# Kernel tuning notes

Measured on AMD Instinct MI355X. Metric: run time of the kernel, lower is better.

## Reference

```python
import jax, jax.numpy as jnp
import numpy as np
import math

F = 64        # num_features (multiplicity of each irrep)
N = 16000     # nodes
E = 256000    # edges (avg_num_neighbors = 16)
S = 4         # num_species
DE = 32       # scalar edge feature dim (radial basis)
W = 128       # interaction_mlp_width
AVG_NEIGH = 16.0
SQ2 = math.sqrt(2.0)
SQ3 = math.sqrt(3.0)


def setup_inputs() -> dict:
    key = jax.random.key(0)
    ks = jax.random.split(key, 32)
    def nrm(k, shape, scale=1.0):
        return jax.random.normal(k, shape, dtype=jnp.float32) * scale
    inp = {}
    # forward args
    inp["vectors"] = nrm(ks[0], (E, 1, 3))
    inp["lengths"] = jax.random.uniform(ks[1], (E, 1), dtype=jnp.float32)
    inp["node_s"] = nrm(ks[2], (N, F))            # 64x0e part of node_feats
    inp["node_v"] = nrm(ks[3], (N, F, 3))         # 64x1o part of node_feats
    inp["scalar_edge_feats"] = nrm(ks[4], (E, DE))
    inp["node_specie"] = jax.random.randint(ks[5], (N,), 0, S)
    inp["senders"] = jax.random.randint(ks[6], (E,), 0, N)
    inp["receivers"] = jax.random.randint(ks[7], (E,), 0, N)
    # parameters (e3nn Linear = per-irrep channel mixing, fan-in normalized; bias only on 0e)
    inp["W_up_s"] = nrm(ks[8], (F, F), F ** -0.5); inp["b_up_s"] = jnp.zeros((F,), jnp.float32)
    inp["W_up_v"] = nrm(ks[9], (F, F), F ** -0.5)
    din = 2 * F + DE + 1
    inp["mlp_W1"] = nrm(ks[10], (din, W), din ** -0.5); inp["mlp_b1"] = jnp.zeros((W,), jnp.float32)
    inp["mlp_W2"] = nrm(ks[11], (W, W), W ** -0.5); inp["mlp_b2"] = jnp.zeros((W,), jnp.float32)
    inp["mlp_W3"] = nrm(ks[12], (W, 3 * F), W ** -0.5); inp["mlp_b3"] = jnp.zeros((3 * F,), jnp.float32)
    inp["W_dn_s"] = nrm(ks[13], (F, F), F ** -0.5); inp["b_dn_s"] = jnp.zeros((F,), jnp.float32)
    inp["W_dn_v"] = nrm(ks[14], (2 * F, F), (2 * F) ** -0.5)
    # symmetric contraction weights (per species, per channel); correlation=2
    inp["w_sc_s"] = nrm(ks[15], (S, 3, F), 3 ** -0.5)   # paths to 0e: x0, x0^2, (x1.x1)/sqrt3
    inp["w_sc_v"] = nrm(ks[16], (S, 2, F), 2 ** -0.5)   # paths to 1o: x1, x0*x1
    inp["W_pb_s"] = nrm(ks[17], (F, F), F ** -0.5); inp["b_pb_s"] = jnp.zeros((F,), jnp.float32)
    inp["W_pb_v"] = nrm(ks[18], (F, F), F ** -0.5)
    inp["W_r1_s"] = nrm(ks[19], (F, 2 * F), F ** -0.5); inp["b_r1_s"] = jnp.zeros((2 * F,), jnp.float32)
    inp["W_r1_v"] = nrm(ks[20], (F, F), F ** -0.5)
    inp["W_r2_s"] = nrm(ks[21], (F, 1), F ** -0.5); inp["b_r2"] = jnp.zeros((1,), jnp.float32)
    inp["W_r2_v"] = nrm(ks[22], (F, 1), F ** -0.5)
    return inp


def reference(vectors, lengths, node_s, node_v, scalar_edge_feats, node_specie,
              senders, receivers,
              W_up_s, b_up_s, W_up_v,
              mlp_W1, mlp_b1, mlp_W2, mlp_b2, mlp_W3, mlp_b3,
              W_dn_s, b_dn_s, W_dn_v,
              w_sc_s, w_sc_v, W_pb_s, b_pb_s, W_pb_v,
              W_r1_s, b_r1_s, W_r1_v, W_r2_s, b_r2, W_r2_v):
    n = node_s.shape[0]
    # --- spherical harmonics, sh_irreps='1o', component normalization, normalize=False ---
    edge_v = SQ3 * vectors[:, 0, :]                              # [E,3]

    # --- InteractionBlock: linear_up ---
    h_s = node_s @ W_up_s + b_up_s                               # [N,F]
    h_v = jnp.einsum('nfi,fg->ngi', node_v, W_up_v)              # [N,F,3]

    # --- MessagePassingConvolution ---
    m_s = h_s[senders]                                           # [E,F] 0e
    m_v = h_v[senders]                                           # [E,F,3] 1o
    # tensor product with edge 1o, filtered to 0e+1o (unitary CG):
    tp_s = jnp.einsum('efi,ei->ef', m_v, edge_v) / SQ3           # 1o x 1o -> 0e  [E,F]
    tp_v1 = m_s[:, :, None] * edge_v[:, None, :]                 # 0e x 1o -> 1o  [E,F,3]
    tp_v2 = jnp.cross(m_v, edge_v[:, None, :]) / SQ2             # 1o x 1o -> 1o  [E,F,3]
    # scalar MLP mix (one scalar weight per output irrep = 3F)
    mlp_in = jnp.concatenate([m_s, h_s[receivers], scalar_edge_feats, lengths], axis=1)
    h = jax.nn.silu(mlp_in @ mlp_W1 + mlp_b1)
    h = jax.nn.silu(h @ mlp_W2 + mlp_b2)
    mix = h @ mlp_W3 + mlp_b3                                    # [E,3F]
    mix_s, mix_v1, mix_v2 = mix[:, :F], mix[:, F:2 * F], mix[:, 2 * F:]
    tp_s = tp_s * mix_s
    tp_v = jnp.concatenate([tp_v1 * mix_v1[:, :, None], tp_v2 * mix_v2[:, :, None]], axis=1)  # [E,2F,3]
    # scatter-add to receivers, normalize by avg_num_neighbors
    agg_s = jax.ops.segment_sum(tp_s, receivers, num_segments=n) / AVG_NEIGH   # [N,F]
    agg_v = jax.ops.segment_sum(tp_v, receivers, num_segments=n) / AVG_NEIGH   # [N,2F,3]
    # linear_down
    f_s = agg_s @ W_dn_s + b_dn_s                                # [N,F]
    f_v = jnp.einsum('nfi,fg->ngi', agg_v, W_dn_v)               # [N,F,3]

    # --- EquivariantProductBasisBlock: symmetric contraction (correlation=2), per-species ---
    ws = w_sc_s[node_specie]                                     # [N,3,F]
    wv = w_sc_v[node_specie]                                     # [N,2,F]
    vv = jnp.sum(f_v * f_v, axis=-1) / SQ3                       # 1o (x) 1o -> 0e, symmetric
    sc_s = ws[:, 0] * f_s + ws[:, 1] * (f_s * f_s) + ws[:, 2] * vv           # [N,F]
    sc_v = wv[:, 0][:, :, None] * f_v + wv[:, 1][:, :, None] * (f_s[:, :, None] * f_v)  # [N,F,3]
    p_s = sc_s @ W_pb_s + b_pb_s                                 # node_feats 0e out
    p_v = jnp.einsum('nfi,fg->ngi', sc_v, W_pb_v)                # node_feats 1o out

    # --- NonLinearReadoutBlock: linear to (2F x 0e + F x 1o), gate, linear to 1x0e+1x1o ---
    r_s = p_s @ W_r1_s + b_r1_s                                  # [N,2F]
    r_v = jnp.einsum('nfi,fg->ngi', p_v, W_r1_v)                 # [N,F,3]
    act = jax.nn.silu(r_s[:, :F])
    gates = jax.nn.silu(r_s[:, F:])
    g_v = gates[:, :, None] * r_v                                # gated vectors
    out_s = act @ W_r2_s + b_r2                                  # [N,1]  0e output
    out_v = jnp.einsum('nfi,fo->noi', g_v, W_r2_v)               # [N,1,3] 1o output
    return out_s, out_v, p_s, p_v
```

## Files before the change

### kernel.cpp

```cpp
#include <hip/hip_runtime.h>

typedef short bf16x8 __attribute__((ext_vector_type(8)));
typedef float f32x4  __attribute__((ext_vector_type(4)));
typedef unsigned short ushort_t;

__device__ __forceinline__ float silu(float x) {
    float t = __expf(-x);
    return x * __builtin_amdgcn_rcpf(1.f + t);
}

__device__ __forceinline__ ushort_t f2bs(float x) {
    union { float f; unsigned int u; } v; v.f = x;
    unsigned int r = v.u + 0x7FFF + ((v.u >> 16) & 1);
    return (ushort_t)(r >> 16);
}
__device__ __forceinline__ ushort_t f2bs_t(float x) {
    union { float f; unsigned int u; } v; v.f = x;
    return (ushort_t)(v.u >> 16);
}
__device__ __forceinline__ float bs2f(ushort_t x) {
    union { unsigned int u; float f; } v; v.u = ((unsigned int)x) << 16; return v.f;
}

constexpr int N_   = 16000;
constexpr int E_   = 256000;
constexpr int Fd   = 64;

constexpr float SQ3f    = 1.7320508075688772f;
constexpr float INV_SQ3 = 0.5773502691896258f;
constexpr float INV_SQ2 = 0.7071067811865476f;
constexpr float INV_AVG = 0.0625f;

constexpr int OFF_OS = 0;
constexpr int OFF_OV = N_;
constexpr int OFF_PS = OFF_OV + 3 * N_;
constexpr int OFF_PV = OFF_PS + N_ * Fd;

constexpr int W1P_SZ = 6 * 8 * 512;
constexpr int W2P_SZ = 4 * 8 * 512;
constexpr int W3P_SZ = 4 * 12 * 512;

__global__ __launch_bounds__(256) void pack_kernel(
    const float* __restrict__ W1, const float* __restrict__ W2,
    const float* __restrict__ W3,
    ushort_t* __restrict__ W1p, ushort_t* __restrict__ W2p,
    ushort_t* __restrict__ W3p)
{
    int idx = blockIdx.x * 256 + threadIdx.x;
    if (idx < W1P_SZ) {
        int j = idx & 7, lane = (idx >> 3) & 63, tile = idx >> 9;
        int c = tile >> 3, t = tile & 7;
        int k = c * 32 + (lane >> 4) * 8 + j;
        int n = t * 16 + (lane & 15);
        W1p[idx] = f2bs(k < 161 ? W1[k * 128 + n] : 0.f);
    } else if (idx < W1P_SZ + W2P_SZ) {
        int q = idx - W1P_SZ;
        int j = q & 7, lane = (q >> 3) & 63, tile = q >> 9;
        int c = tile >> 3, t = tile & 7;
        int k = c * 32 + (lane >> 4) * 8 + j;
        int n = t * 16 + (lane & 15);
        W2p[q] = f2bs(W2[k * 128 + n]);
    } else {
        int q = idx - W1P_SZ - W2P_SZ;
        int j = q & 7, lane = (q >> 3) & 63, tile = q >> 9;
        int c = tile / 12, t = tile % 12;
        int k = c * 32 + (lane >> 4) * 8 + j;
        int n = t * 16 + (lane & 15);
        W3p[q] = f2bs(W3[k * 192 + n]);
    }
}

__global__ __launch_bounds__(64, 4) void up_kernel(
    const float* __restrict__ node_s, const float* __restrict__ node_v,
    const float* __restrict__ W_up_s, const float* __restrict__ b_up_s,
    const float* __restrict__ W_up_v,
    const int* __restrict__ receivers, int* __restrict__ cnt,
    ushort_t* __restrict__ hs_bf, float* __restrict__ h_v)
{
    __shared__ float ns[4][64];
    __shared__ float nv[4][64][3];
    const int n0 = blockIdx.x * 4;
    const int g  = threadIdx.x;

    {
        int e = blockIdx.x * 64 + g;
        atomicAdd(&cnt[receivers[e]], 1);
    }

    #pragma unroll
    for (int j = 0; j < 4; j++) ns[j][g] = node_s[(n0 + j) * 64 + g];
    for (int idx = g; idx < 4 * 192; idx += 64) {
        int j = idx / 192, r = idx - j * 192;
        nv[j][r / 3][r % 3] = node_v[(size_t)n0 * 192 + idx];
    }
    __syncthreads();

    float as[4], a0[4], a1[4], a2[4];
    float bb = b_up_s[g];
    #pragma unroll
    for (int j = 0; j < 4; j++) { as[j] = bb; a0[j] = a1[j] = a2[j] = 0.f; }
    #pragma unroll 4
    for (int f = 0; f < 64; f++) {
        float wss = W_up_s[f * 64 + g];
        float wv  = W_up_v[f * 64 + g];
        #pragma unroll
        for (int j = 0; j < 4; j++) {
            as[j] += ns[j][f] * wss;
            a0[j] += nv[j][f][0] * wv;
            a1[j] += nv[j][f][1] * wv;
            a2[j] += nv[j][f][2] * wv;
        }
    }
    #pragma unroll
    for (int j = 0; j < 4; j++) {
        hs_bf[(n0 + j) * 64 + g] = f2bs(as[j]);
        h_v[(n0 + j) * 192 + 0 * 64 + g] = a0[j];
        h_v[(n0 + j) * 192 + 1 * 64 + g] = a1[j];
        h_v[(n0 + j) * 192 + 2 * 64 + g] = a2[j];
    }
}

__global__ __launch_bounds__(1024) void scan_kernel(
    const int* __restrict__ cnt, int* __restrict__ base, int* __restrict__ cursor)
{
    __shared__ int part[1024];
    const int t = threadIdx.x;
    int v[16];
    int s = 0;
    if (t < 1000) {
        const int4* c4 = (const int4*)(cnt + t * 16);
        #pragma unroll
        for (int q = 0; q < 4; q++) {
            int4 w = c4[q];
            v[q * 4 + 0] = w.x; v[q * 4 + 1] = w.y;
            v[q * 4 + 2] = w.z; v[q * 4 + 3] = w.w;
            s += w.x + w.y + w.z + w.w;
        }
    }
    part[t] = s;
    __syncthreads();
    for (int off = 1; off < 1024; off <<= 1) {
        int u = (t >= off) ? part[t - off] : 0;
        __syncthreads();
        part[t] += u;
        __syncthreads();
    }
    if (t < 1000) {
        int run = part[t] - s;
        int b[16];
        #pragma unroll
        for (int i = 0; i < 16; i++) { b[i] = run; run += v[i]; }
        int4* bb = (int4*)(base + t * 16);
        int4* cc = (int4*)(cursor + t * 16);
        #pragma unroll
        for (int q = 0; q < 4; q++) {
            int4 w = { b[q * 4], b[q * 4 + 1], b[q * 4 + 2], b[q * 4 + 3] };
            bb[q] = w;
            cc[q] = w;
        }
    }
}

__global__ __launch_bounds__(256, 3) void edge_mlp_kernel(
    const float* __restrict__ lengths, const float* __restrict__ sef,
    const int* __restrict__ senders, const int* __restrict__ receivers,
    const float* __restrict__ vectors,
    const float* __restrict__ b1f, const float* __restrict__ b2f,
    const float* __restrict__ b3f,
    const ushort_t* __restrict__ hs_bf,
    const ushort_t* __restrict__ W1p, const ushort_t* __restrict__ W2p,
    const ushort_t* __restrict__ W3p,
    int* __restrict__ cursor, float4* __restrict__ meta,
    ushort_t* __restrict__ tpx)
{
    __shared__ ushort_t Als[64 * 200];
    __shared__ ushort_t Hs[64 * 136];
    __shared__ int perm_s[64];

    const int tid  = threadIdx.x;
    const int wave = tid >> 6, lane = tid & 63;
    const int quad = lane >> 4, l4 = lane & 15;
    const int e0   = blockIdx.x * 64;

    if (tid < 64) {
        int e = e0 + tid;
        int p = atomicAdd(&cursor[receivers[e]], 1);
        perm_s[tid] = p;
        float4 mt;
        mt.x = __int_as_float(senders[e]);
        mt.y = SQ3f * vectors[e * 3 + 0];
        mt.z = SQ3f * vectors[e * 3 + 1];
        mt.w = SQ3f * vectors[e * 3 + 2];
        meta[p] = mt;
    }

    {
        const int e  = tid & 63;
        const int ge = e0 + e;
        const int snd = senders[ge];
        const int rcv = receivers[ge];
        for (int c = tid >> 6; c < 24; c += 4) {
            bf16x8 v;
            if (c < 8) {
                v = *(const bf16x8*)(hs_bf + snd * 64 + c * 8);
            } else if (c < 16) {
                v = *(const bf16x8*)(hs_bf + rcv * 64 + (c - 8) * 8);
            } else if (c < 20) {
                const float4 s0 = *(const float4*)(sef + (size_t)ge * 32 + (c - 16) * 8);
                const float4 s1 = *(const float4*)(sef + (size_t)ge * 32 + (c - 16) * 8 + 4);
                v[0] = (short)f2bs(s0.x); v[1] = (short)f2bs(s0.y);
                v[2] = (short)f2bs(s0.z); v[3] = (short)f2bs(s0.w);
                v[4] = (short)f2bs(s1.x); v[5] = (short)f2bs(s1.y);
                v[6] = (short)f2bs(s1.z); v[7] = (short)f2bs(s1.w);
            } else if (c == 20) {
                v = (bf16x8){0,0,0,0,0,0,0,0};
                v[0] = (short)f2bs(lengths[ge]);
            } else {
                v = (bf16x8){0,0,0,0,0,0,0,0};
            }
            *(bf16x8*)(&Als[e * 200 + c * 8]) = v;
        }
    }
    __syncthreads();

    const bf16x8* B1 = (const bf16x8*)W1p;
    const bf16x8* B2 = (const bf16x8*)W2p;
    const bf16x8* B3 = (const bf16x8*)W3p;

    {
        f32x4 acc[2][4];
        #pragma unroll
        for (int ti = 0; ti < 2; ti++)
            #pragma unroll
            for (int m = 0; m < 4; m++) acc[ti][m] = (f32x4){0,0,0,0};
        #pragma unroll
        for (int c = 0; c < 6; c++) {
            bf16x8 b0 = B1[(c * 8 + wave * 2 + 0) * 64 + lane];
            bf16x8 b1 = B1[(c * 8 + wave * 2 + 1) * 64 + lane];
            #pragma unroll
            for (int m = 0; m < 4; m++) {
                bf16x8 a = *(const bf16x8*)(&Als[(m * 16 + l4) * 200 + c * 32 + quad * 8]);
                acc[0][m] = __builtin_amdgcn_mfma_f32_16x16x32_bf16(a, b0, acc[0][m], 0, 0, 0);
                acc[1][m] = __builtin_amdgcn_mfma_f32_16x16x32_bf16(a, b1, acc[1][m], 0, 0, 0);
            }
        }
        #pragma unroll
        for (int ti = 0; ti < 2; ti++) {
            int t = wave * 2 + ti;
            float bb = b1f[t * 16 + l4];
            #pragma unroll
            for (int m = 0; m < 4; m++)
                #pragma unroll
                for (int r = 0; r < 4; r++)
                    Hs[(m * 16 + quad * 4 + r) * 136 + t * 16 + l4] =
                        f2bs_t(silu(acc[ti][m][r] + bb));
        }
    }
    __syncthreads();

    {
        f32x4 acc[2][4];
        #pragma unroll
        for (int ti = 0; ti < 2; ti++)
            #pragma unroll
            for (int m = 0; m < 4; m++) acc[ti][m] = (f32x4){0,0,0,0};
        #pragma unroll
        for (int c = 0; c < 4; c++) {
            bf16x8 b0 = B2[(c * 8 + wave * 2 + 0) * 64 + lane];
            bf16x8 b1 = B2[(c * 8 + wave * 2 + 1) * 64 + lane];
            #pragma unroll
            for (int m = 0; m < 4; m++) {
                bf16x8 a = *(const bf16x8*)(&Hs[(m * 16 + l4) * 136 + c * 32 + quad * 8]);
                acc[0][m] = __builtin_amdgcn_mfma_f32_16x16x32_bf16(a, b0, acc[0][m], 0, 0, 0);
                acc[1][m] = __builtin_amdgcn_mfma_f32_16x16x32_bf16(a, b1, acc[1][m], 0, 0, 0);
            }
        }
        #pragma unroll
        for (int ti = 0; ti < 2; ti++) {
            int t = wave * 2 + ti;
            float bb = b2f[t * 16 + l4];
            #pragma unroll
            for (int m = 0; m < 4; m++)
                #pragma unroll
                for (int r = 0; r < 4; r++)
                    Als[(m * 16 + quad * 4 + r) * 136 + t * 16 + l4] =
                        f2bs_t(silu(acc[ti][m][r] + bb));
        }
    }
    __syncthreads();

    {
        f32x4 acc[3][4];
        #pragma unroll
        for (int ti = 0; ti < 3; ti++)
            #pragma unroll
            for (int m = 0; m < 4; m++) acc[ti][m] = (f32x4){0,0,0,0};
        #pragma unroll
        for (int c = 0; c < 4; c++) {
            bf16x8 b0 = B3[(c * 12 + wave * 3 + 0) * 64 + lane];
            bf16x8 b1 = B3[(c * 12 + wave * 3 + 1) * 64 + lane];
            bf16x8 b2 = B3[(c * 12 + wave * 3 + 2) * 64 + lane];
            #pragma unroll
            for (int m = 0; m < 4; m++) {
                bf16x8 a = *(const bf16x8*)(&Als[(m * 16 + l4) * 136 + c * 32 + quad * 8]);
                acc[0][m] = __builtin_amdgcn_mfma_f32_16x16x32_bf16(a, b0, acc[0][m], 0, 0, 0);
                acc[1][m] = __builtin_amdgcn_mfma_f32_16x16x32_bf16(a, b1, acc[1][m], 0, 0, 0);
                acc[2][m] = __builtin_amdgcn_mfma_f32_16x16x32_bf16(a, b2, acc[2][m], 0, 0, 0);
            }
        }
        #pragma unroll
        for (int ti = 0; ti < 3; ti++) {
            int t = wave * 3 + ti;
            float bb = b3f[t * 16 + l4];
            #pragma unroll
            for (int m = 0; m < 4; m++)
                #pragma unroll
                for (int r = 0; r < 4; r++) {
                    int p = perm_s[m * 16 + quad * 4 + r];
                    tpx[(size_t)p * 192 + t * 16 + l4] = f2bs(acc[ti][m][r] + bb);
                }
        }
    }
}

__global__ __launch_bounds__(256, 2) void node_fused_kernel(
    const int* __restrict__ base, const int* __restrict__ cnt,
    const float4* __restrict__ meta,
    const ushort_t* __restrict__ tpx,
    const ushort_t* __restrict__ hs_bf, const float* __restrict__ h_v,
    const int* __restrict__ specie,
    const float* __restrict__ W_dn_s, const float* __restrict__ b_dn_s,
    const float* __restrict__ W_dn_v,
    const float* __restrict__ w_sc_s, const float* __restrict__ w_sc_v,
    const float* __restrict__ W_pb_s, const float* __restrict__ b_pb_s,
    const float* __restrict__ W_pb_v,
    const float* __restrict__ W_r1_s, const float* __restrict__ b_r1_s,
    const float* __restrict__ W_r1_v,
    const float* __restrict__ W_r2_s, const float* __restrict__ b_r2,
    const float* __restrict__ W_r2_v,
    float* __restrict__ out)
{
    __shared__ float as_l[4][64];
    __shared__ float av_l[4][128][3];
    __shared__ float scs[4][64];
    __shared__ float scv[4][64][3];
    __shared__ float ps_[4][64];
    __shared__ float pv_[4][64][3];
    __shared__ float4 lmeta[4][64];

    const int tid = threadIdx.x;
    const int w   = tid >> 6;
    const int g   = tid & 63;
    const int n   = blockIdx.x * 4 + w;

    const int b = base[n];
    const int c = cnt[n];
    float accSa = 0.f, accSb = 0.f;
    float a10a = 0.f, a11a = 0.f, a12a = 0.f;
    float a20a = 0.f, a21a = 0.f, a22a = 0.f;
    float a10b = 0.f, a11b = 0.f, a12b = 0.f;
    float a20b = 0.f, a21b = 0.f, a22b = 0.f;

    for (int done = 0; done < c; done += 64) {
        int m = min(64, c - done);
        if (g < m) lmeta[w][g] = meta[b + done + g];
        int i = 0;
        for (; i + 1 < m; i += 2) {
            const float4 mt1 = lmeta[w][i];
            const float4 mt2 = lmeta[w][i + 1];
            const int se1 = __float_as_int(mt1.x);
            const int se2 = __float_as_int(mt2.x);
            const float ev10 = mt1.y, ev11 = mt1.z, ev12 = mt1.w;
            const float ev20 = mt2.y, ev21 = mt2.z, ev22 = mt2.w;
            const float m10 = h_v[(size_t)se1 * 192 + 0 * 64 + g];
            const float m11 = h_v[(size_t)se1 * 192 + 1 * 64 + g];
            const float m12 = h_v[(size_t)se1 * 192 + 2 * 64 + g];
            const float m20 = h_v[(size_t)se2 * 192 + 0 * 64 + g];
            const float m21 = h_v[(size_t)se2 * 192 + 1 * 64 + g];
            const float m22 = h_v[(size_t)se2 * 192 + 2 * 64 + g];
            const float ms1 = bs2f(hs_bf[se1 * 64 + g]);
            const float ms2 = bs2f(hs_bf[se2 * 64 + g]);
            const ushort_t* r1 = tpx + (size_t)(b + done + i) * 192;
            const ushort_t* r2 = r1 + 192;
            const float c10 = bs2f(r1[g]), c11 = bs2f(r1[64 + g]), c12 = bs2f(r1[128 + g]);
            const float c20 = bs2f(r2[g]), c21 = bs2f(r2[64 + g]), c22 = bs2f(r2[128 + g]);

            accSa += (m10 * ev10 + m11 * ev11 + m12 * ev12) * c10;
            accSb += (m20 * ev20 + m21 * ev21 + m22 * ev22) * c20;
            float k1a = ms1 * c11, k1b = ms2 * c21;
            a10a += k1a * ev10; a11a += k1a * ev11; a12a += k1a * ev12;
            a10b += k1b * ev20; a11b += k1b * ev21; a12b += k1b * ev22;
            a20a += (m11 * ev12 - m12 * ev11) * c12;
            a21a += (m12 * ev10 - m10 * ev12) * c12;
            a22a += (m10 * ev11 - m11 * ev10) * c12;
            a20b += (m21 * ev22 - m22 * ev21) * c22;
            a21b += (m22 * ev20 - m20 * ev22) * c22;
            a22b += (m20 * ev21 - m21 * ev20) * c22;
        }
        if (i < m) {
            const float4 mt1 = lmeta[w][i];
            const int se1 = __float_as_int(mt1.x);
            const float ev10 = mt1.y, ev11 = mt1.z, ev12 = mt1.w;
            const float m10 = h_v[(size_t)se1 * 192 + 0 * 64 + g];
            const float m11 = h_v[(size_t)se1 * 192 + 1 * 64 + g];
            const float m12 = h_v[(size_t)se1 * 192 + 2 * 64 + g];
            const float ms1 = bs2f(hs_bf[se1 * 64 + g]);
            const ushort_t* r1 = tpx + (size_t)(b + done + i) * 192;
            const float c10 = bs2f(r1[g]), c11 = bs2f(r1[64 + g]), c12 = bs2f(r1[128 + g]);
            accSa += (m10 * ev10 + m11 * ev11 + m12 * ev12) * c10;
            float k1a = ms1 * c11;
            a10a += k1a * ev10; a11a += k1a * ev11; a12a += k1a * ev12;
            a20a += (m11 * ev12 - m12 * ev11) * c12;
            a21a += (m12 * ev10 - m10 * ev12) * c12;
            a22a += (m10 * ev11 - m11 * ev10) * c12;
        }
    }
    as_l[w][g] = (accSa + accSb) * (INV_SQ3 * INV_AVG);
    av_l[w][g][0] = (a10a + a10b) * INV_AVG;
    av_l[w][g][1] = (a11a + a11b) * INV_AVG;
    av_l[w][g][2] = (a12a + a12b) * INV_AVG;
    av_l[w][64 + g][0] = (a20a + a20b) * (INV_SQ2 * INV_AVG);
    av_l[w][64 + g][1] = (a21a + a21b) * (INV_SQ2 * INV_AVG);
    av_l[w][64 + g][2] = (a22a + a22b) * (INV_SQ2 * INV_AVG);

    float f_s = b_dn_s[g];
    #pragma unroll 8
    for (int f = 0; f < 64; f++) f_s += as_l[w][f] * W_dn_s[f * 64 + g];
    float fv0 = 0.f, fv1 = 0.f, fv2 = 0.f;
    #pragma unroll 8
    for (int f = 0; f < 128; f++) {
        float wt = W_dn_v[f * 64 + g];
        fv0 += av_l[w][f][0] * wt;
        fv1 += av_l[w][f][1] * wt;
        fv2 += av_l[w][f][2] * wt;
    }

    float vv = (fv0 * fv0 + fv1 * fv1 + fv2 * fv2) * INV_SQ3;
    int sp = specie[n];
    float ws0 = w_sc_s[sp * 192 + 0 * 64 + g];
    float ws1 = w_sc_s[sp * 192 + 1 * 64 + g];
    float ws2 = w_sc_s[sp * 192 + 2 * 64 + g];
    float wv0 = w_sc_v[sp * 128 + 0 * 64 + g];
    float wv1 = w_sc_v[sp * 128 + 1 * 64 + g];
    float sc_s = ws0 * f_s + ws1 * f_s * f_s + ws2 * vv;
    float kv = wv0 + wv1 * f_s;
    scs[w][g] = sc_s;
    scv[w][g][0] = kv * fv0;
    scv[w][g][1] = kv * fv1;
    scv[w][g][2] = kv * fv2;

    float p_s = b_pb_s[g];
    float pv0 = 0.f, pv1 = 0.f, pv2 = 0.f;
    #pragma unroll 8
    for (int f = 0; f < 64; f++) {
        float wps = W_pb_s[f * 64 + g];
        p_s += scs[w][f] * wps;
        float wpv = W_pb_v[f * 64 + g];
        pv0 += scv[w][f][0] * wpv;
        pv1 += scv[w][f][1] * wpv;
        pv2 += scv[w][f][2] * wpv;
    }
    ps_[w][g] = p_s;
    pv_[w][g][0] = pv0; pv_[w][g][1] = pv1; pv_[w][g][2] = pv2;

    out[OFF_PS + n * 64 + g] = p_s;
    out[OFF_PV + (size_t)n * 192 + g * 3 + 0] = pv0;
    out[OFF_PV + (size_t)n * 192 + g * 3 + 1] = pv1;
    out[OFF_PV + (size_t)n * 192 + g * 3 + 2] = pv2;

    float r0 = b_r1_s[g];
    float r1 = b_r1_s[g + 64];
    float rv0 = 0.f, rv1 = 0.f, rv2 = 0.f;
    #pragma unroll 8
    for (int f = 0; f < 64; f++) {
        float p = ps_[w][f];
        r0 += p * W_r1_s[f * 128 + g];
        r1 += p * W_r1_s[f * 128 + g + 64];
        float wrv = W_r1_v[f * 64 + g];
        rv0 += pv_[w][f][0] * wrv;
        rv1 += pv_[w][f][1] * wrv;
        rv2 += pv_[w][f][2] * wrv;
    }
    float act  = silu(r0);
    float gate = silu(r1);
    float o_s = act * W_r2_s[g];
    float wr2v = W_r2_v[g];
    float ov0 = gate * rv0 * wr2v;
    float ov1 = gate * rv1 * wr2v;
    float ov2 = gate * rv2 * wr2v;

    #pragma unroll
    for (int off = 32; off > 0; off >>= 1) {
        o_s += __shfl_down(o_s, off);
        ov0 += __shfl_down(ov0, off);
        ov1 += __shfl_down(ov1, off);
        ov2 += __shfl_down(ov2, off);
    }
    if (g == 0) {
        out[OFF_OS + n] = o_s + b_r2[0];
        out[OFF_OV + n * 3 + 0] = ov0;
        out[OFF_OV + n * 3 + 1] = ov1;
        out[OFF_OV + n * 3 + 2] = ov2;
    }
}

extern "C" void kernel_launch(void* const* d_in, const int* in_sizes, int n_in,
                              void* d_out, int out_size, void* d_ws, size_t ws_size,
                              hipStream_t stream)
{
    const float* vectors  = (const float*)d_in[0];
    const float* lengths  = (const float*)d_in[1];
    const float* node_s   = (const float*)d_in[2];
    const float* node_v   = (const float*)d_in[3];
    const float* sef      = (const float*)d_in[4];
    const int*  specie    = (const int*)d_in[5];
    const int*  senders   = (const int*)d_in[6];
    const int*  receivers = (const int*)d_in[7];
    const float* W_up_s   = (const float*)d_in[8];
    const float* b_up_s   = (const float*)d_in[9];
    const float* W_up_v   = (const float*)d_in[10];
    const float* mlp_W1   = (const float*)d_in[11];
    const float* mlp_b1   = (const float*)d_in[12];
    const float* mlp_W2   = (const float*)d_in[13];
    const float* mlp_b2   = (const float*)d_in[14];
    const float* mlp_W3   = (const float*)d_in[15];
    const float* mlp_b3   = (const float*)d_in[16];
    const float* W_dn_s   = (const float*)d_in[17];
    const float* b_dn_s   = (const float*)d_in[18];
    const float* W_dn_v   = (const float*)d_in[19];
    const float* w_sc_s   = (const float*)d_in[20];
    const float* w_sc_v   = (const float*)d_in[21];
    const float* W_pb_s   = (const float*)d_in[22];
    const float* b_pb_s   = (const float*)d_in[23];
    const float* W_pb_v   = (const float*)d_in[24];
    const float* W_r1_s   = (const float*)d_in[25];
    const float* b_r1_s   = (const float*)d_in[26];
    const float* W_r1_v   = (const float*)d_in[27];
    const float* W_r2_s   = (const float*)d_in[28];
    const float* b_r2     = (const float*)d_in[29];
    const float* W_r2_v   = (const float*)d_in[30];

    float* h_v = (float*)d_ws;
    ushort_t* tpx   = (ushort_t*)(h_v + (size_t)N_ * 192);
    ushort_t* hs_bf = tpx + (size_t)E_ * 192;
    ushort_t* W1p   = hs_bf + (size_t)N_ * 64;
    ushort_t* W2p   = W1p + W1P_SZ;
    ushort_t* W3p   = W2p + W2P_SZ;
    float4* meta    = (float4*)((((size_t)(W3p + W3P_SZ)) + 15) & ~(size_t)15);
    int* cnt        = (int*)(meta + E_);
    int* base       = cnt + N_;
    int* cursor     = base + N_;

    float* out = (float*)d_out;

    hipMemsetAsync(cnt, 0, N_ * sizeof(int), stream);

    up_kernel<<<N_ / 4, 64, 0, stream>>>(node_s, node_v, W_up_s, b_up_s, W_up_v,
                                         receivers, cnt, hs_bf, h_v);
    pack_kernel<<<256, 256, 0, stream>>>(mlp_W1, mlp_W2, mlp_W3, W1p, W2p, W3p);
    scan_kernel<<<1, 1024, 0, stream>>>(cnt, base, cursor);

    edge_mlp_kernel<<<E_ / 64, 256, 0, stream>>>(
        lengths, sef, senders, receivers, vectors,
        mlp_b1, mlp_b2, mlp_b3,
        hs_bf, W1p, W2p, W3p, cursor, meta, tpx);

    node_fused_kernel<<<N_ / 4, 256, 0, stream>>>(
        base, cnt, meta,
        tpx, hs_bf, h_v, specie,
        W_dn_s, b_dn_s, W_dn_v, w_sc_s, w_sc_v,
        W_pb_s, b_pb_s, W_pb_v, W_r1_s, b_r1_s, W_r1_v,
        W_r2_s, b_r2, W_r2_v, out);
}
```

Measured before the change: 364.4 us.

## Pack sender features and edge weights into interleaved bf16 layouts for gathers

The sender vector features h_v move from fp32 to bf16 and are interleaved with the scalar feature into one uint2 per channel, so the node kernel does a single 8-byte gather per sender instead of three fp32 loads and a bf16 load. The edge MLP output is split into an interleaved pair (components 0 and 1 packed in a uint) plus a separate component-2 array. It is staged through shared memory so the permuted scatter writes full 16-byte rows instead of scattered 2-byte stores. This cuts gather traffic and store inefficiency, but lowers h_v precision to bf16 and adds an extra LDS pass and barriers in the edge kernel.

Measured after the change: 375.4 us. 3.0% more time.

```diff
diff --git a/kernel.cpp b/kernel.cpp
--- a/kernel.cpp
+++ b/kernel.cpp
@@ -3,6 +3,7 @@
 typedef short bf16x8 __attribute__((ext_vector_type(8)));
 typedef float f32x4  __attribute__((ext_vector_type(4)));
 typedef unsigned short ushort_t;
+typedef unsigned int uint_t;
 
 __device__ __forceinline__ float silu(float x) {
     float t = __expf(-x);
@@ -75,7 +76,7 @@
     const float* __restrict__ W_up_s, const float* __restrict__ b_up_s,
     const float* __restrict__ W_up_v,
     const int* __restrict__ receivers, int* __restrict__ cnt,
-    ushort_t* __restrict__ hs_bf, float* __restrict__ h_v)
+    ushort_t* __restrict__ hs_bf, uint2* __restrict__ hvp)
 {
     __shared__ float ns[4][64];
     __shared__ float nv[4][64][3];
@@ -114,9 +115,9 @@
     #pragma unroll
     for (int j = 0; j < 4; j++) {
         hs_bf[(n0 + j) * 64 + g] = f2bs(as[j]);
-        h_v[(n0 + j) * 192 + 0 * 64 + g] = a0[j];
-        h_v[(n0 + j) * 192 + 1 * 64 + g] = a1[j];
-        h_v[(n0 + j) * 192 + 2 * 64 + g] = a2[j];
+        uint_t lo = (uint_t)f2bs(a0[j]) | ((uint_t)f2bs(a1[j]) << 16);
+        uint_t hi = (uint_t)f2bs(a2[j]) | ((uint_t)f2bs(as[j]) << 16);
+        hvp[(size_t)(n0 + j) * 64 + g] = make_uint2(lo, hi);
     }
 }
 
@@ -171,11 +172,12 @@
     const ushort_t* __restrict__ W1p, const ushort_t* __restrict__ W2p,
     const ushort_t* __restrict__ W3p,
     int* __restrict__ cursor, float4* __restrict__ meta,
-    ushort_t* __restrict__ tpx)
+    uint_t* __restrict__ tpA, ushort_t* __restrict__ tpB)
 {
-    __shared__ ushort_t Als[64 * 200];
-    __shared__ ushort_t Hs[64 * 136];
+    __shared__ ushort_t SMEM[64 * 200 + 64 * 136];
     __shared__ int perm_s[64];
+    ushort_t* Als = SMEM;
+    ushort_t* Hs  = SMEM + 64 * 200;
 
     const int tid  = threadIdx.x;
     const int wave = tid >> 6, lane = tid & 63;
@@ -289,45 +291,69 @@
     }
     __syncthreads();
 
+    f32x4 acc3[3][4];
+    #pragma unroll
+    for (int ti = 0; ti < 3; ti++)
+        #pragma unroll
+        for (int m = 0; m < 4; m++) acc3[ti][m] = (f32x4){0,0,0,0};
+    #pragma unroll
+    for (int c = 0; c < 4; c++) {
+        bf16x8 b0 = B3[(c * 12 + wave * 3 + 0) * 64 + lane];
+        bf16x8 b1 = B3[(c * 12 + wave * 3 + 1) * 64 + lane];
+        bf16x8 b2 = B3[(c * 12 + wave * 3 + 2) * 64 + lane];
+        #pragma unroll
+        for (int m = 0; m < 4; m++) {
+            bf16x8 a = *(const bf16x8*)(&Als[(m * 16 + l4) * 136 + c * 32 + quad * 8]);
+            acc3[0][m] = __builtin_amdgcn_mfma_f32_16x16x32_bf16(a, b0, acc3[0][m], 0, 0, 0);
+            acc3[1][m] = __builtin_amdgcn_mfma_f32_16x16x32_bf16(a, b1, acc3[1][m], 0, 0, 0);
+            acc3[2][m] = __builtin_amdgcn_mfma_f32_16x16x32_bf16(a, b2, acc3[2][m], 0, 0, 0);
+        }
+    }
+    __syncthreads();
+
     {
-        f32x4 acc[3][4];
-        #pragma unroll
-        for (int ti = 0; ti < 3; ti++)
-            #pragma unroll
-            for (int m = 0; m < 4; m++) acc[ti][m] = (f32x4){0,0,0,0};
-        #pragma unroll
-        for (int c = 0; c < 4; c++) {
-            bf16x8 b0 = B3[(c * 12 + wave * 3 + 0) * 64 + lane];
-            bf16x8 b1 = B3[(c * 12 + wave * 3 + 1) * 64 + lane];
-            bf16x8 b2 = B3[(c * 12 + wave * 3 + 2) * 64 + lane];
-            #pragma unroll
-            for (int m = 0; m < 4; m++) {
-                bf16x8 a = *(const bf16x8*)(&Als[(m * 16 + l4) * 136 + c * 32 + quad * 8]);
-                acc[0][m] = __builtin_amdgcn_mfma_f32_16x16x32_bf16(a, b0, acc[0][m], 0, 0, 0);
-                acc[1][m] = __builtin_amdgcn_mfma_f32_16x16x32_bf16(a, b1, acc[1][m], 0, 0, 0);
-                acc[2][m] = __builtin_amdgcn_mfma_f32_16x16x32_bf16(a, b2, acc[2][m], 0, 0, 0);
-            }
-        }
+        ushort_t* Lm16 = SMEM;
+        ushort_t* Lc2  = SMEM + 8192;
         #pragma unroll
         for (int ti = 0; ti < 3; ti++) {
             int t = wave * 3 + ti;
+            int comp = t >> 2, fb = t & 3;
             float bb = b3f[t * 16 + l4];
+            int f = fb * 16 + l4;
             #pragma unroll
             for (int m = 0; m < 4; m++)
                 #pragma unroll
                 for (int r = 0; r < 4; r++) {
-                    int p = perm_s[m * 16 + quad * 4 + r];
-                    tpx[(size_t)p * 192 + t * 16 + l4] = f2bs(acc[ti][m][r] + bb);
+                    int row = m * 16 + quad * 4 + r;
+                    ushort_t v = f2bs(acc3[ti][m][r] + bb);
+                    if (comp == 2) Lc2[row * 64 + f] = v;
+                    else           Lm16[(row * 64 + f) * 2 + comp] = v;
                 }
         }
+    }
+    __syncthreads();
+
+    {
+        const uint_t* Lm32 = (const uint_t*)SMEM;
+        const ushort_t* Lc2 = SMEM + 8192;
+        int row = tid >> 2, q = tid & 3;
+        size_t p = (size_t)perm_s[row];
+        const uint4* srcA = (const uint4*)(Lm32 + row * 64 + q * 16);
+        uint4* dstA = (uint4*)(tpA + p * 64 + q * 16);
+        #pragma unroll
+        for (int k = 0; k < 4; k++) dstA[k] = srcA[k];
+        const uint4* srcB = (const uint4*)(Lc2 + row * 64 + q * 16);
+        uint4* dstB = (uint4*)(tpB + p * 64 + q * 16);
+        dstB[0] = srcB[0];
+        dstB[1] = srcB[1];
     }
 }
 
 __global__ __launch_bounds__(256, 2) void node_fused_kernel(
     const int* __restrict__ base, const int* __restrict__ cnt,
     const float4* __restrict__ meta,
-    const ushort_t* __restrict__ tpx,
-    const ushort_t* __restrict__ hs_bf, const float* __restrict__ h_v,
+    const uint_t* __restrict__ tpA, const ushort_t* __restrict__ tpB,
+    const uint2* __restrict__ hvp,
     const int* __restrict__ specie,
     const float* __restrict__ W_dn_s, const float* __restrict__ b_dn_s,
     const float* __restrict__ W_dn_v,
@@ -370,20 +396,28 @@
             const float4 mt2 = lmeta[w][i + 1];
             const int se1 = __float_as_int(mt1.x);
             const int se2 = __float_as_int(mt2.x);
+            const uint2 h1 = hvp[(size_t)se1 * 64 + g];
+            const uint2 h2 = hvp[(size_t)se2 * 64 + g];
+            const uint_t t1 = tpA[(size_t)(b + done + i) * 64 + g];
+            const uint_t t2 = tpA[(size_t)(b + done + i + 1) * 64 + g];
+            const float c12 = bs2f(tpB[(size_t)(b + done + i) * 64 + g]);
+            const float c22 = bs2f(tpB[(size_t)(b + done + i + 1) * 64 + g]);
+
+            const float m10 = __uint_as_float(h1.x << 16);
+            const float m11 = __uint_as_float(h1.x & 0xffff0000u);
+            const float m12 = __uint_as_float(h1.y << 16);
+            const float ms1 = __uint_as_float(h1.y & 0xffff0000u);
+            const float m20 = __uint_as_float(h2.x << 16);
+            const float m21 = __uint_as_float(h2.x & 0xffff0000u);
+            const float m22 = __uint_as_float(h2.y << 16);
+            const float ms2 = __uint_as_float(h2.y & 0xffff0000u);
+            const float c10 = __uint_as_float(t1 << 16);
+            const float c11 = __uint_as_float(t1 & 0xffff0000u);
+            const float c20 = __uint_as_float(t2 << 16);
+            const float c21 = __uint_as_float(t2 & 0xffff0000u);
+
             const float ev10 = mt1.y, ev11 = mt1.z, ev12 = mt1.w;
             const float ev20 = mt2.y, ev21 = mt2.z, ev22 = mt2.w;
-            const float m10 = h_v[(size_t)se1 * 192 + 0 * 64 + g];
-            const float m11 = h_v[(size_t)se1 * 192 + 1 * 64 + g];
-            const float m12 = h_v[(size_t)se1 * 192 + 2 * 64 + g];
-            const float m20 = h_v[(size_t)se2 * 192 + 0 * 64 + g];
-            const float m21 = h_v[(size_t)se2 * 192 + 1 * 64 + g];
-            const float m22 = h_v[(size_t)se2 * 192 + 2 * 64 + g];
-            const float ms1 = bs2f(hs_bf[se1 * 64 + g]);
-            const float ms2 = bs2f(hs_bf[se2 * 64 + g]);
-            const ushort_t* r1 = tpx + (size_t)(b + done + i) * 192;
-            const ushort_t* r2 = r1 + 192;
-            const float c10 = bs2f(r1[g]), c11 = bs2f(r1[64 + g]), c12 = bs2f(r1[128 + g]);
-            const float c20 = bs2f(r2[g]), c21 = bs2f(r2[64 + g]), c22 = bs2f(r2[128 + g]);
 
             accSa += (m10 * ev10 + m11 * ev11 + m12 * ev12) * c10;
             accSb += (m20 * ev20 + m21 * ev21 + m22 * ev22) * c20;
@@ -400,13 +434,16 @@
         if (i < m) {
             const float4 mt1 = lmeta[w][i];
             const int se1 = __float_as_int(mt1.x);
+            const uint2 h1 = hvp[(size_t)se1 * 64 + g];
+            const uint_t t1 = tpA[(size_t)(b + done + i) * 64 + g];
+            const float c12 = bs2f(tpB[(size_t)(b + done + i) * 64 + g]);
+            const float m10 = __uint_as_float(h1.x << 16);
+            const float m11 = __uint_as_float(h1.x & 0xffff0000u);
+            const float m12 = __uint_as_float(h1.y << 16);
+            const float ms1 = __uint_as_float(h1.y & 0xffff0000u);
+            const float c10 = __uint_as_float(t1 << 16);
+            const float c11 = __uint_as_float(t1 & 0xffff0000u);
             const float ev10 = mt1.y, ev11 = mt1.z, ev12 = mt1.w;
-            const float m10 = h_v[(size_t)se1 * 192 + 0 * 64 + g];
-            const float m11 = h_v[(size_t)se1 * 192 + 1 * 64 + g];
-            const float m12 = h_v[(size_t)se1 * 192 + 2 * 64 + g];
-            const float ms1 = bs2f(hs_bf[se1 * 64 + g]);
-            const ushort_t* r1 = tpx + (size_t)(b + done + i) * 192;
-            const float c10 = bs2f(r1[g]), c11 = bs2f(r1[64 + g]), c12 = bs2f(r1[128 + g]);
             accSa += (m10 * ev10 + m11 * ev11 + m12 * ev12) * c10;
             float k1a = ms1 * c11;
             a10a += k1a * ev10; a11a += k1a * ev11; a12a += k1a * ev12;
@@ -540,14 +577,15 @@
     const float* b_r2     = (const float*)d_in[29];
     const float* W_r2_v   = (const float*)d_in[30];
 
-    float* h_v = (float*)d_ws;
-    ushort_t* tpx   = (ushort_t*)(h_v + (size_t)N_ * 192);
-    ushort_t* hs_bf = tpx + (size_t)E_ * 192;
+    float4*   meta  = (float4*)d_ws;
+    uint_t*   tpA   = (uint_t*)(meta + E_);
+    ushort_t* tpB   = (ushort_t*)(tpA + (size_t)E_ * 64);
+    uint2*    hvp   = (uint2*)(tpB + (size_t)E_ * 64);
+    ushort_t* hs_bf = (ushort_t*)(hvp + (size_t)N_ * 64);
     ushort_t* W1p   = hs_bf + (size_t)N_ * 64;
     ushort_t* W2p   = W1p + W1P_SZ;
     ushort_t* W3p   = W2p + W2P_SZ;
-    float4* meta    = (float4*)((((size_t)(W3p + W3P_SZ)) + 15) & ~(size_t)15);
-    int* cnt        = (int*)(meta + E_);
+    int* cnt        = (int*)((((size_t)(W3p + W3P_SZ)) + 15) & ~(size_t)15);
     int* base       = cnt + N_;
     int* cursor     = base + N_;
 
@@ -556,18 +594,17 @@
     hipMemsetAsync(cnt, 0, N_ * sizeof(int), stream);
 
     up_kernel<<<N_ / 4, 64, 0, stream>>>(node_s, node_v, W_up_s, b_up_s, W_up_v,
-                                         receivers, cnt, hs_bf, h_v);
+                                         receivers, cnt, hs_bf, hvp);
     pack_kernel<<<256, 256, 0, stream>>>(mlp_W1, mlp_W2, mlp_W3, W1p, W2p, W3p);
     scan_kernel<<<1, 1024, 0, stream>>>(cnt, base, cursor);
 
     edge_mlp_kernel<<<E_ / 64, 256, 0, stream>>>(
         lengths, sef, senders, receivers, vectors,
         mlp_b1, mlp_b2, mlp_b3,
-        hs_bf, W1p, W2p, W3p, cursor, meta, tpx);
+        hs_bf, W1p, W2p, W3p, cursor, meta, tpA, tpB);
 
     node_fused_kernel<<<N_ / 4, 256, 0, stream>>>(
-        base, cnt, meta,
-        tpx, hs_bf, h_v, specie,
+        base, cnt, meta, tpA, tpB, hvp, specie,
         W_dn_s, b_dn_s, W_dn_v, w_sc_s, w_sc_v,
         W_pb_s, b_pb_s, W_pb_v, W_r1_s, b_r1_s, W_r1_v,
         W_r2_s, b_r2, W_r2_v, out);
```
